# Kernel tuning notes

Hardware: AMD Instinct MI355X
Metric: run time of the kernel (lower is better)

Reference implementation:

```python
import jax, jax.numpy as jnp
import numpy as np

B, H, W, C = 8, 128, 128, 128
HEADS = 4
KSIZE = 7  # neighborhood kernel size


def setup_inputs() -> dict:
    key = jax.random.key(0)
    ks = jax.random.split(key, 8)
    def nrm(k, shape, scale=0.02):
        return jax.random.normal(k, shape, jnp.float32) * scale
    return {
        "x": jax.random.normal(ks[0], (B, H, W, C), jnp.float32),
        "norm1_w": jnp.ones((C,), jnp.float32),
        "norm1_b": jnp.zeros((C,), jnp.float32),
        "qkv_w": nrm(ks[1], (3 * C, C)),
        "qkv_b": jnp.zeros((3 * C,), jnp.float32),
        "rpb": nrm(ks[2], (HEADS, 2 * KSIZE - 1)),
        "proj_w": nrm(ks[3], (C, C)),
        "proj_b": jnp.zeros((C,), jnp.float32),
        "norm2_w": jnp.ones((C,), jnp.float32),
        "norm2_b": jnp.zeros((C,), jnp.float32),
        "fc1_w": nrm(ks[4], (4 * C, C)),
        "fc1_b": jnp.zeros((4 * C,), jnp.float32),
        "fc2_w": nrm(ks[5], (C, 4 * C)),
        "fc2_b": jnp.zeros((C,), jnp.float32),
    }


def layer_norm(x, w, b, eps=1e-5):
    mu = x.mean(-1, keepdims=True)
    var = ((x - mu) ** 2).mean(-1, keepdims=True)
    return (x - mu) * jax.lax.rsqrt(var + eps) * w + b


def reference(x, norm1_w, norm1_b, qkv_w, qkv_b, rpb, proj_w, proj_b,
              norm2_w, norm2_b, fc1_w, fc1_b, fc2_w, fc2_b):
    B_, H_, W_, C_ = x.shape
    N = H_ * W_
    h = HEADS
    d = C_ // h
    k = KSIZE

    shortcut = x
    xs = layer_norm(x, norm1_w, norm1_b).reshape(B_, N, C_)

    # --- 1D neighborhood attention over the flattened (row-major) sequence ---
    qkv = xs @ qkv_w.T + qkv_b                      # (B, N, 3C)
    q, kk, v = jnp.split(qkv, 3, axis=-1)
    q = q.reshape(B_, N, h, d) * (d ** -0.5)
    kk = kk.reshape(B_, N, h, d)
    v = v.reshape(B_, N, h, d)

    pos = jnp.arange(N)
    starts = jnp.clip(pos - k // 2, 0, N - k)       # clamped window start (NATTEN-style)
    nbr = starts[:, None] + jnp.arange(k)           # (N, k) neighbor indices

    k_g = kk[:, nbr]                                # (B, N, k, h, d)
    v_g = v[:, nbr]                                 # (B, N, k, h, d)

    logits = jnp.einsum('bnhd,bnkhd->bhnk', q, k_g)  # (B, h, N, k)
    bias_idx = nbr - pos[:, None] + (k - 1)          # in [0, 2k-2]
    logits = logits + rpb[:, bias_idx]               # (h, N, k) broadcast over B
    attn = jax.nn.softmax(logits, axis=-1)

    out = jnp.einsum('bhnk,bnkhd->bnhd', attn, v_g).reshape(B_, N, C_)
    out = out @ proj_w.T + proj_b

    x = shortcut + out.reshape(B_, H_, W_, C_)

    # --- MLP block ---
    y = layer_norm(x, norm2_w, norm2_b)
    y = jax.nn.gelu(y @ fc1_w.T + fc1_b, approximate=False)
    y = y @ fc2_w.T + fc2_b
    return x + y
```

## Files before the change

kernel.cpp:

```cpp
#include <hip/hip_runtime.h>
#include <hip/hip_bf16.h>


#define NPOS 16384
#define MROWS 131072

typedef unsigned short ushort_t;
typedef __bf16 bf8 __attribute__((ext_vector_type(8)));
typedef float f4 __attribute__((ext_vector_type(4)));

#define P_QKV_W 0
#define P_QKV_B 49152
#define P_PROJ_W 49536
#define P_PROJ_B 65920
#define P_FC1_W 66048
#define P_FC1_B 131584
#define P_FC2_W 132096
#define P_FC2_B 197632
#define P_TOTAL 197760

__device__ __forceinline__ float b2f(ushort_t u) {
    union { unsigned int i; float f; } v; v.i = ((unsigned int)u) << 16; return v.f;
}
__device__ __forceinline__ ushort_t f2b(float f) {
    __hip_bfloat16 h = __float2bfloat16(f);
    return *reinterpret_cast<ushort_t*>(&h);
}
__device__ __forceinline__ int swz(int row, int col, int stride) {
    return row * stride + ((((col >> 3) ^ ((row >> 2) & 3)) << 3) | (col & 7));
}
__device__ __forceinline__ int swz8(int row, int col) {
    return row * 128 + ((((col >> 3) ^ (row & 7)) << 3) | (col & 7));
}
__device__ __forceinline__ void ld8(const ushort_t* p, float* d) {
    uint4 pv = *(const uint4*)p;
    const ushort_t* us = (const ushort_t*)&pv;
    #pragma unroll
    for (int e = 0; e < 8; e++) d[e] = b2f(us[e]);
}
__device__ __forceinline__ void st8(ushort_t* p, const float* d) {
    unsigned int pk[4];
    #pragma unroll
    for (int e = 0; e < 4; e++)
        pk[e] = (unsigned int)f2b(d[2 * e]) | ((unsigned int)f2b(d[2 * e + 1]) << 16);
    *(uint4*)p = *(uint4*)pk;
}
__device__ __forceinline__ float fast_gelu(float x) {
    float u = x * (0.7978845608f + 0.0356774081f * x * x);
    float t = 1.0f - 2.0f / (1.0f + __expf(2.0f * u));
    return 0.5f * x * (1.0f + t);
}

__global__ __launch_bounds__(256) void cvt_params(
    const float* __restrict__ qkv_w, const float* __restrict__ qkv_b,
    const float* __restrict__ proj_w, const float* __restrict__ proj_b,
    const float* __restrict__ fc1_w, const float* __restrict__ fc1_b,
    const float* __restrict__ fc2_w, const float* __restrict__ fc2_b,
    ushort_t* __restrict__ p)
{
    int i = blockIdx.x * 256 + threadIdx.x;
    if (i >= P_TOTAL) return;
    float v;
    if      (i < P_QKV_B)  v = qkv_w[i - P_QKV_W];
    else if (i < P_PROJ_W) v = qkv_b[i - P_QKV_B];
    else if (i < P_PROJ_B) v = proj_w[i - P_PROJ_W];
    else if (i < P_FC1_W)  v = proj_b[i - P_PROJ_B];
    else if (i < P_FC1_B)  v = fc1_w[i - P_FC1_W];
    else if (i < P_FC2_W)  v = fc1_b[i - P_FC1_B];
    else if (i < P_FC2_B)  v = fc2_w[i - P_FC2_W];
    else                   v = fc2_b[i - P_FC2_B];
    p[i] = f2b(v);
}

__global__ __launch_bounds__(512, 2) void k_fused(
    const float* __restrict__ x, const float* __restrict__ n1w,
    const float* __restrict__ n1b, const ushort_t* __restrict__ qkvw,
    const float* __restrict__ qkvb, const float* __restrict__ rpb,
    const ushort_t* __restrict__ projw, const float* __restrict__ projb,
    const float* __restrict__ n2w, const float* __restrict__ n2b,
    const ushort_t* __restrict__ fc1w, const float* __restrict__ fc1b,
    const ushort_t* __restrict__ fc2w, const float* __restrict__ fc2b,
    float* __restrict__ out)
{
    extern __shared__ ushort_t sm[];
    ushort_t* xs   = sm;
    ushort_t* kv   = sm + 10240;
    ushort_t* xres = sm + 31360;
    ushort_t* qo   = sm;
    ushort_t* ct   = sm + 10240;
    ushort_t* ys   = sm;
    ushort_t* h    = sm + 18944;

    int t0  = blockIdx.x * 64;
    int ib  = t0 & ~(NPOS - 1);
    int nl0 = t0 & (NPOS - 1);
    int tid = threadIdx.x;
    int w = tid >> 6, lane = tid & 63;
    int quad = lane >> 4, lrow = lane & 15;

    {
        int grp = tid >> 4, l = tid & 15;
        int c0 = l * 8;
        float4 wa = *(const float4*)&n1w[c0], wb = *(const float4*)&n1w[c0 + 4];
        float4 ba = *(const float4*)&n1b[c0], bb = *(const float4*)&n1b[c0 + 4];
        float w8[8] = {wa.x, wa.y, wa.z, wa.w, wb.x, wb.y, wb.z, wb.w};
        float b8[8] = {ba.x, ba.y, ba.z, ba.w, bb.x, bb.y, bb.z, bb.w};
        #pragma unroll
        for (int pass = 0; pass < 3; pass++) {
            int r = pass * 32 + grp;
            if (r < 80) {
                int nl = min(max(nl0 - 8 + r, 0), NPOS - 1);
                const float* xp = &x[(size_t)(ib + nl) * 128 + c0];
                float4 va = *(const float4*)xp;
                float4 vb = *(const float4*)(xp + 4);
                float v[8] = {va.x, va.y, va.z, va.w, vb.x, vb.y, vb.z, vb.w};
                float s = 0.f, s2 = 0.f;
                #pragma unroll
                for (int e = 0; e < 8; e++) { s += v[e]; s2 += v[e] * v[e]; }
                #pragma unroll
                for (int off = 8; off; off >>= 1) {
                    s  += __shfl_xor(s,  off, 64);
                    s2 += __shfl_xor(s2, off, 64);
                }
                float mu   = s * (1.0f / 128.0f);
                float rstd = rsqrtf(s2 * (1.0f / 128.0f) - mu * mu + 1e-5f);
                float o[8];
                #pragma unroll
                for (int e = 0; e < 8; e++) o[e] = (v[e] - mu) * rstd * w8[e] + b8[e];
                st8(&xs[swz8(r, c0)], o);
                if (r >= 8 && r < 72) st8(&xres[swz(r - 8, c0, 136)], v);
            }
        }
    }
    __syncthreads();

    {
        f4 acc[5][3];
        #pragma unroll
        for (int i = 0; i < 5; i++)
            #pragma unroll
            for (int j = 0; j < 3; j++) { f4 z = {0.f,0.f,0.f,0.f}; acc[i][j] = z; }
        #pragma unroll
        for (int k0 = 0; k0 < 128; k0 += 32) {
            bf8 bv[3];
            #pragma unroll
            for (int jj = 0; jj < 3; jj++) {
                int n = (3 * w + jj) * 16 + lrow;
                bv[jj] = *(const bf8*)&qkvw[(size_t)n * 128 + k0 + quad * 8];
            }
            #pragma unroll
            for (int i = 0; i < 5; i++) {
                bf8 av = *(const bf8*)&xs[swz8(i * 16 + lrow, k0 + quad * 8)];
                #pragma unroll
                for (int jj = 0; jj < 3; jj++)
                    acc[i][jj] = __builtin_amdgcn_mfma_f32_16x16x32_bf16(
                        av, bv[jj], acc[i][jj], 0, 0, 0);
            }
        }
        __syncthreads();
        #pragma unroll
        for (int jj = 0; jj < 3; jj++) {
            int jt = 3 * w + jj;
            int n = jt * 16 + lrow;
            float bj = qkvb[n];
            #pragma unroll
            for (int i = 0; i < 5; i++) {
                #pragma unroll
                for (int r = 0; r < 4; r++) {
                    int mrow = i * 16 + quad * 4 + r;
                    float v = acc[i][jj][r] + bj;
                    if (jt < 8) {
                        if (mrow >= 8 && mrow < 72)
                            qo[swz(mrow - 8, n, 136)] = f2b(v * 0.17677669529663687f);
                    } else {
                        kv[swz(mrow, n - 128, 264)] = f2b(v);
                    }
                }
            }
        }
    }
    __syncthreads();

    {
        int t = tid >> 3, head = (tid >> 1) & 3, half = tid & 1;
        int n = nl0 + t;
        int s = n - 3;
        if (s < 0) s = 0;
        if (s > NPOS - 7) s = NPOS - 7;
        int r0 = s - nl0 + 8;
        int cb = head * 32 + half * 16;

        float q[16];
        ld8(&qo[swz(t, cb, 136)], q);
        ld8(&qo[swz(t, cb + 8, 136)], q + 8);

        float logit[7];
        #pragma unroll
        for (int j = 0; j < 7; j++) {
            int row = r0 + j;
            float kk[8];
            float p = 0.f;
            ld8(&kv[swz(row, cb, 264)], kk);
            #pragma unroll
            for (int e = 0; e < 8; e++) p += q[e] * kk[e];
            ld8(&kv[swz(row, cb + 8, 264)], kk);
            #pragma unroll
            for (int e = 0; e < 8; e++) p += q[8 + e] * kk[e];
            p += __shfl_xor(p, 1, 64);
            logit[j] = p + rpb[head * 13 + (s + j - n + 6)];
        }
        float m = logit[0];
        #pragma unroll
        for (int j = 1; j < 7; j++) m = fmaxf(m, logit[j]);
        float e[7], esum = 0.f;
        #pragma unroll
        for (int j = 0; j < 7; j++) { e[j] = __expf(logit[j] - m); esum += e[j]; }
        float inv = 1.0f / esum;

        float o[16];
        #pragma unroll
        for (int c = 0; c < 16; c++) o[c] = 0.f;
        #pragma unroll
        for (int j = 0; j < 7; j++) {
            int row = r0 + j;
            float vv[8];
            float ej = e[j];
            ld8(&kv[swz(row, 128 + cb, 264)], vv);
            #pragma unroll
            for (int c = 0; c < 8; c++) o[c] += ej * vv[c];
            ld8(&kv[swz(row, 128 + cb + 8, 264)], vv);
            #pragma unroll
            for (int c = 0; c < 8; c++) o[8 + c] += ej * vv[c];
        }
        #pragma unroll
        for (int c = 0; c < 16; c++) o[c] *= inv;
        st8(&qo[swz(t, cb, 136)], o);
        st8(&qo[swz(t, cb + 8, 136)], o + 8);
    }
    __syncthreads();

    {
        int n = w * 16 + lrow;
        f4 acc2[4];
        #pragma unroll
        for (int i = 0; i < 4; i++) { f4 z = {0.f,0.f,0.f,0.f}; acc2[i] = z; }
        #pragma unroll
        for (int k0 = 0; k0 < 128; k0 += 32) {
            bf8 bv = *(const bf8*)&projw[(size_t)n * 128 + k0 + quad * 8];
            #pragma unroll
            for (int i = 0; i < 4; i++) {
                bf8 av = *(const bf8*)&qo[swz(i * 16 + lrow, k0 + quad * 8, 136)];
                acc2[i] = __builtin_amdgcn_mfma_f32_16x16x32_bf16(av, bv, acc2[i], 0, 0, 0);
            }
        }
        float bj = projb[n];
        #pragma unroll
        for (int i = 0; i < 4; i++) {
            #pragma unroll
            for (int r = 0; r < 4; r++) {
                int row = i * 16 + quad * 4 + r;
                float v = acc2[i][r] + bj + b2f(xres[swz(row, n, 136)]);
                ct[swz(row, n, 136)] = f2b(v);
            }
        }
    }
    __syncthreads();

    {
        int grp = tid >> 4, l = tid & 15;
        int c0 = l * 8;
        float4 wa = *(const float4*)&n2w[c0], wb = *(const float4*)&n2w[c0 + 4];
        float4 ba = *(const float4*)&n2b[c0], bb = *(const float4*)&n2b[c0 + 4];
        float w8[8] = {wa.x, wa.y, wa.z, wa.w, wb.x, wb.y, wb.z, wb.w};
        float b8[8] = {ba.x, ba.y, ba.z, ba.w, bb.x, bb.y, bb.z, bb.w};
        #pragma unroll
        for (int pass = 0; pass < 2; pass++) {
            int t = pass * 32 + grp;
            float v[8];
            ld8(&ct[swz(t, c0, 136)], v);
            float s = 0.f, s2 = 0.f;
            #pragma unroll
            for (int e = 0; e < 8; e++) { s += v[e]; s2 += v[e] * v[e]; }
            #pragma unroll
            for (int off = 8; off; off >>= 1) {
                s  += __shfl_xor(s,  off, 64);
                s2 += __shfl_xor(s2, off, 64);
            }
            float mu   = s * (1.0f / 128.0f);
            float rstd = rsqrtf(s2 * (1.0f / 128.0f) - mu * mu + 1e-5f);
            float o[8];
            #pragma unroll
            for (int e = 0; e < 8; e++) o[e] = (v[e] - mu) * rstd * w8[e] + b8[e];
            st8(&ys[swz(t, c0, 136)], o);
        }
    }
    __syncthreads();

    {
        f4 acc2[4];
        #pragma unroll
        for (int i = 0; i < 4; i++) { f4 z = {0.f,0.f,0.f,0.f}; acc2[i] = z; }
        int n = w * 16 + lrow;

        for (int hh = 0; hh < 2; hh++) {
            f4 acc[4][2];
            #pragma unroll
            for (int i = 0; i < 4; i++)
                #pragma unroll
                for (int j = 0; j < 2; j++) { f4 z = {0.f,0.f,0.f,0.f}; acc[i][j] = z; }
            #pragma unroll
            for (int k0 = 0; k0 < 128; k0 += 32) {
                bf8 bv[2];
                #pragma unroll
                for (int jj = 0; jj < 2; jj++) {
                    int frow = hh * 256 + (w * 2 + jj) * 16 + lrow;
                    bv[jj] = *(const bf8*)&fc1w[(size_t)frow * 128 + k0 + quad * 8];
                }
                #pragma unroll
                for (int i = 0; i < 4; i++) {
                    bf8 av = *(const bf8*)&ys[swz(i * 16 + lrow, k0 + quad * 8, 136)];
                    #pragma unroll
                    for (int jj = 0; jj < 2; jj++)
                        acc[i][jj] = __builtin_amdgcn_mfma_f32_16x16x32_bf16(
                            av, bv[jj], acc[i][jj], 0, 0, 0);
                }
            }
            __syncthreads();
            #pragma unroll
            for (int jj = 0; jj < 2; jj++) {
                int cb = (w * 2 + jj) * 16 + lrow;
                float bj = fc1b[hh * 256 + cb];
                #pragma unroll
                for (int i = 0; i < 4; i++) {
                    #pragma unroll
                    for (int r = 0; r < 4; r++) {
                        int row = i * 16 + quad * 4 + r;
                        h[swz(row, cb, 264)] = f2b(fast_gelu(acc[i][jj][r] + bj));
                    }
                }
            }
            __syncthreads();
            #pragma unroll
            for (int k0 = 0; k0 < 256; k0 += 32) {
                bf8 bv = *(const bf8*)&fc2w[(size_t)n * 512 + hh * 256 + k0 + quad * 8];
                #pragma unroll
                for (int i = 0; i < 4; i++) {
                    bf8 av = *(const bf8*)&h[swz(i * 16 + lrow, k0 + quad * 8, 264)];
                    acc2[i] = __builtin_amdgcn_mfma_f32_16x16x32_bf16(av, bv, acc2[i], 0, 0, 0);
                }
            }
        }

        float bj = fc2b[n];
        #pragma unroll
        for (int i = 0; i < 4; i++) {
            #pragma unroll
            for (int r = 0; r < 4; r++) {
                int row = i * 16 + quad * 4 + r;
                out[(size_t)(t0 + row) * 128 + n] =
                    acc2[i][r] + bj + b2f(ct[swz(row, n, 136)]);
            }
        }
    }
}

extern "C" void kernel_launch(void* const* d_in, const int* in_sizes, int n_in,
                              void* d_out, int out_size, void* d_ws, size_t ws_size,
                              hipStream_t stream) {
    const float* x      = (const float*)d_in[0];
    const float* n1w    = (const float*)d_in[1];
    const float* n1b    = (const float*)d_in[2];
    const float* qkv_w  = (const float*)d_in[3];
    const float* qkv_b  = (const float*)d_in[4];
    const float* rpb    = (const float*)d_in[5];
    const float* proj_w = (const float*)d_in[6];
    const float* proj_b = (const float*)d_in[7];
    const float* n2w    = (const float*)d_in[8];
    const float* n2b    = (const float*)d_in[9];
    const float* fc1_w  = (const float*)d_in[10];
    const float* fc1_b  = (const float*)d_in[11];
    const float* fc2_w  = (const float*)d_in[12];
    const float* fc2_b  = (const float*)d_in[13];

    ushort_t* params = (ushort_t*)d_ws;
    float*    outf   = (float*)d_out;

    cvt_params<<<(P_TOTAL + 255) / 256, 256, 0, stream>>>(
        qkv_w, qkv_b, proj_w, proj_b, fc1_w, fc1_b, fc2_w, fc2_b, params);

    k_fused<<<MROWS / 64, 512, 80128, stream>>>(
        x, n1w, n1b, params + P_QKV_W, qkv_b, rpb,
        params + P_PROJ_W, proj_b, n2w, n2b,
        params + P_FC1_W, fc1_b, params + P_FC2_W, fc2_b, outf);
}
```

Baseline: 342.0 us.

## Shrink LDS footprint by trimming halo and keeping residuals in registers

Cuts the halo rows from 8 to 3 on each side (70 rows instead of 80) and drops the padded-stride swizzle in favour of XOR swizzles with power-of-two strides. It also stops staging the residual x in LDS: x is reread from global memory into registers before the projection, and the post-attention residual is kept in registers for the final output instead of being read back from LDS. Shared memory per block falls from about 80KB to about 54KB and launch bounds go from 2 to 6, aiming for more resident blocks per CU. The cost is more register pressure and an extra global read of x, plus an added barrier before ct is written, since ct now aliases the kv region.

```diff
diff --git a/kernel.cpp b/kernel.cpp
--- a/kernel.cpp
+++ b/kernel.cpp
@@ -1,6 +1,5 @@
 #include <hip/hip_runtime.h>
 #include <hip/hip_bf16.h>
-
 
 #define NPOS 16384
 #define MROWS 131072
@@ -26,11 +25,11 @@
     __hip_bfloat16 h = __float2bfloat16(f);
     return *reinterpret_cast<ushort_t*>(&h);
 }
-__device__ __forceinline__ int swz(int row, int col, int stride) {
-    return row * stride + ((((col >> 3) ^ ((row >> 2) & 3)) << 3) | (col & 7));
-}
 __device__ __forceinline__ int swz8(int row, int col) {
     return row * 128 + ((((col >> 3) ^ (row & 7)) << 3) | (col & 7));
+}
+__device__ __forceinline__ int swzK(int row, int col) {
+    return row * 256 + ((((col >> 3) ^ (row & 7)) << 3) | (col & 7));
 }
 __device__ __forceinline__ void ld8(const ushort_t* p, float* d) {
     uint4 pv = *(const uint4*)p;
@@ -72,7 +71,7 @@
     p[i] = f2b(v);
 }
 
-__global__ __launch_bounds__(512, 2) void k_fused(
+__global__ __launch_bounds__(512, 6) void k_fused(
     const float* __restrict__ x, const float* __restrict__ n1w,
     const float* __restrict__ n1b, const ushort_t* __restrict__ qkvw,
     const float* __restrict__ qkvb, const float* __restrict__ rpb,
@@ -83,13 +82,12 @@
     float* __restrict__ out)
 {
     extern __shared__ ushort_t sm[];
-    ushort_t* xs   = sm;
-    ushort_t* kv   = sm + 10240;
-    ushort_t* xres = sm + 31360;
-    ushort_t* qo   = sm;
-    ushort_t* ct   = sm + 10240;
-    ushort_t* ys   = sm;
-    ushort_t* h    = sm + 18944;
+    ushort_t* xs = sm;
+    ushort_t* kv = sm + 8960;
+    ushort_t* qo = sm;
+    ushort_t* ct = sm + 8960;
+    ushort_t* ys = sm;
+    ushort_t* h  = sm + 8960;
 
     int t0  = blockIdx.x * 64;
     int ib  = t0 & ~(NPOS - 1);
@@ -108,8 +106,8 @@
         #pragma unroll
         for (int pass = 0; pass < 3; pass++) {
             int r = pass * 32 + grp;
-            if (r < 80) {
-                int nl = min(max(nl0 - 8 + r, 0), NPOS - 1);
+            if (r < 70) {
+                int nl = min(max(nl0 - 3 + r, 0), NPOS - 1);
                 const float* xp = &x[(size_t)(ib + nl) * 128 + c0];
                 float4 va = *(const float4*)xp;
                 float4 vb = *(const float4*)(xp + 4);
@@ -128,7 +126,6 @@
                 #pragma unroll
                 for (int e = 0; e < 8; e++) o[e] = (v[e] - mu) * rstd * w8[e] + b8[e];
                 st8(&xs[swz8(r, c0)], o);
-                if (r >= 8 && r < 72) st8(&xres[swz(r - 8, c0, 136)], v);
             }
         }
     }
@@ -167,13 +164,14 @@
             for (int i = 0; i < 5; i++) {
                 #pragma unroll
                 for (int r = 0; r < 4; r++) {
-                    int mrow = i * 16 + quad * 4 + r;
+                    int g = i * 16 + quad * 4 + r;
                     float v = acc[i][jj][r] + bj;
                     if (jt < 8) {
-                        if (mrow >= 8 && mrow < 72)
-                            qo[swz(mrow - 8, n, 136)] = f2b(v * 0.17677669529663687f);
+                        if (g >= 3 && g < 67)
+                            qo[swz8(g - 3, n)] = f2b(v * 0.17677669529663687f);
                     } else {
-                        kv[swz(mrow, n - 128, 264)] = f2b(v);
+                        if (g < 70)
+                            kv[swzK(g, n - 128)] = f2b(v);
                     }
                 }
             }
@@ -187,12 +185,12 @@
         int s = n - 3;
         if (s < 0) s = 0;
         if (s > NPOS - 7) s = NPOS - 7;
-        int r0 = s - nl0 + 8;
+        int r0 = s - nl0 + 3;
         int cb = head * 32 + half * 16;
 
         float q[16];
-        ld8(&qo[swz(t, cb, 136)], q);
-        ld8(&qo[swz(t, cb + 8, 136)], q + 8);
+        ld8(&qo[swz8(t, cb)], q);
+        ld8(&qo[swz8(t, cb + 8)], q + 8);
 
         float logit[7];
         #pragma unroll
@@ -200,10 +198,10 @@
             int row = r0 + j;
             float kk[8];
             float p = 0.f;
-            ld8(&kv[swz(row, cb, 264)], kk);
+            ld8(&kv[swzK(row, cb)], kk);
             #pragma unroll
             for (int e = 0; e < 8; e++) p += q[e] * kk[e];
-            ld8(&kv[swz(row, cb + 8, 264)], kk);
+            ld8(&kv[swzK(row, cb + 8)], kk);
             #pragma unroll
             for (int e = 0; e < 8; e++) p += q[8 + e] * kk[e];
             p += __shfl_xor(p, 1, 64);
@@ -225,22 +223,29 @@
             int row = r0 + j;
             float vv[8];
             float ej = e[j];
-            ld8(&kv[swz(row, 128 + cb, 264)], vv);
+            ld8(&kv[swzK(row, 128 + cb)], vv);
             #pragma unroll
             for (int c = 0; c < 8; c++) o[c] += ej * vv[c];
-            ld8(&kv[swz(row, 128 + cb + 8, 264)], vv);
+            ld8(&kv[swzK(row, 128 + cb + 8)], vv);
             #pragma unroll
             for (int c = 0; c < 8; c++) o[8 + c] += ej * vv[c];
         }
         #pragma unroll
         for (int c = 0; c < 16; c++) o[c] *= inv;
-        st8(&qo[swz(t, cb, 136)], o);
-        st8(&qo[swz(t, cb + 8, 136)], o + 8);
+        st8(&qo[swz8(t, cb)], o);
+        st8(&qo[swz8(t, cb + 8)], o + 8);
     }
     __syncthreads();
 
+    float res[16];
     {
         int n = w * 16 + lrow;
+        float xr[16];
+        #pragma unroll
+        for (int i = 0; i < 4; i++)
+            #pragma unroll
+            for (int r = 0; r < 4; r++)
+                xr[i * 4 + r] = x[(size_t)(t0 + i * 16 + quad * 4 + r) * 128 + n];
         f4 acc2[4];
         #pragma unroll
         for (int i = 0; i < 4; i++) { f4 z = {0.f,0.f,0.f,0.f}; acc2[i] = z; }
@@ -249,18 +254,20 @@
             bf8 bv = *(const bf8*)&projw[(size_t)n * 128 + k0 + quad * 8];
             #pragma unroll
             for (int i = 0; i < 4; i++) {
-                bf8 av = *(const bf8*)&qo[swz(i * 16 + lrow, k0 + quad * 8, 136)];
+                bf8 av = *(const bf8*)&qo[swz8(i * 16 + lrow, k0 + quad * 8)];
                 acc2[i] = __builtin_amdgcn_mfma_f32_16x16x32_bf16(av, bv, acc2[i], 0, 0, 0);
             }
         }
         float bj = projb[n];
+        __syncthreads();
         #pragma unroll
         for (int i = 0; i < 4; i++) {
             #pragma unroll
             for (int r = 0; r < 4; r++) {
                 int row = i * 16 + quad * 4 + r;
-                float v = acc2[i][r] + bj + b2f(xres[swz(row, n, 136)]);
-                ct[swz(row, n, 136)] = f2b(v);
+                float v = acc2[i][r] + bj + xr[i * 4 + r];
+                res[i * 4 + r] = v;
+                ct[swz8(row, n)] = f2b(v);
             }
         }
     }
@@ -277,7 +284,7 @@
         for (int pass = 0; pass < 2; pass++) {
             int t = pass * 32 + grp;
             float v[8];
-            ld8(&ct[swz(t, c0, 136)], v);
+            ld8(&ct[swz8(t, c0)], v);
             float s = 0.f, s2 = 0.f;
             #pragma unroll
             for (int e = 0; e < 8; e++) { s += v[e]; s2 += v[e] * v[e]; }
@@ -291,7 +298,7 @@
             float o[8];
             #pragma unroll
             for (int e = 0; e < 8; e++) o[e] = (v[e] - mu) * rstd * w8[e] + b8[e];
-            st8(&ys[swz(t, c0, 136)], o);
+            st8(&ys[swz8(t, c0)], o);
         }
     }
     __syncthreads();
@@ -318,7 +325,7 @@
                 }
                 #pragma unroll
                 for (int i = 0; i < 4; i++) {
-                    bf8 av = *(const bf8*)&ys[swz(i * 16 + lrow, k0 + quad * 8, 136)];
+                    bf8 av = *(const bf8*)&ys[swz8(i * 16 + lrow, k0 + quad * 8)];
                     #pragma unroll
                     for (int jj = 0; jj < 2; jj++)
                         acc[i][jj] = __builtin_amdgcn_mfma_f32_16x16x32_bf16(
@@ -335,7 +342,7 @@
                     #pragma unroll
                     for (int r = 0; r < 4; r++) {
                         int row = i * 16 + quad * 4 + r;
-                        h[swz(row, cb, 264)] = f2b(fast_gelu(acc[i][jj][r] + bj));
+                        h[swzK(row, cb)] = f2b(fast_gelu(acc[i][jj][r] + bj));
                     }
                 }
             }
@@ -345,7 +352,7 @@
                 bf8 bv = *(const bf8*)&fc2w[(size_t)n * 512 + hh * 256 + k0 + quad * 8];
                 #pragma unroll
                 for (int i = 0; i < 4; i++) {
-                    bf8 av = *(const bf8*)&h[swz(i * 16 + lrow, k0 + quad * 8, 264)];
+                    bf8 av = *(const bf8*)&h[swzK(i * 16 + lrow, k0 + quad * 8)];
                     acc2[i] = __builtin_amdgcn_mfma_f32_16x16x32_bf16(av, bv, acc2[i], 0, 0, 0);
                 }
             }
@@ -356,9 +363,8 @@
         for (int i = 0; i < 4; i++) {
             #pragma unroll
             for (int r = 0; r < 4; r++) {
-                int row = i * 16 + quad * 4 + r;
-                out[(size_t)(t0 + row) * 128 + n] =
-                    acc2[i][r] + bj + b2f(ct[swz(row, n, 136)]);
+                int grow = t0 + i * 16 + quad * 4 + r;
+                out[(size_t)grow * 128 + n] = acc2[i][r] + bj + res[i * 4 + r];
             }
         }
     }
@@ -388,7 +394,7 @@
     cvt_params<<<(P_TOTAL + 255) / 256, 256, 0, stream>>>(
         qkv_w, qkv_b, proj_w, proj_b, fc1_w, fc1_b, fc2_w, fc2_b, params);
 
-    k_fused<<<MROWS / 64, 512, 80128, stream>>>(
+    k_fused<<<MROWS / 64, 512, 53760, stream>>>(
         x, n1w, n1b, params + P_QKV_W, qkv_b, rpb,
         params + P_PROJ_W, proj_b, n2w, n2b,
         params + P_FC1_W, fc1_b, params + P_FC2_W, fc2_b, outf);
```

Result: slower. 626.2 us (+83.1%).
